# Optimization experiments

Hardware: AMD Instinct MI355X
Metric: run time of the kernel (lower is better)

## Reference

```python
import jax, jax.numpy as jnp
import numpy as np

N_NODES = 50000
N_EDGES = 800000


def setup_inputs() -> dict:
    key = jax.random.key(0)
    ks = jax.random.split(key, 8)
    x = jax.random.normal(ks[0], (N_NODES, 128), dtype=jnp.float32)
    edge_index = jax.random.randint(ks[1], (2, N_EDGES), 0, N_NODES, dtype=jnp.int64)
    # Glorot-ish scaled weights (GCNConv uses glorot init)
    W1 = jax.random.normal(ks[2], (128, 128), dtype=jnp.float32) * 0.08
    W2 = jax.random.normal(ks[3], (128, 128), dtype=jnp.float32) * 0.08
    W3 = jax.random.normal(ks[4], (128, 64), dtype=jnp.float32) * 0.08
    b1 = jnp.zeros((128,), jnp.float32)
    b2 = jnp.zeros((128,), jnp.float32)
    b3 = jnp.zeros((64,), jnp.float32)
    return {"x": x, "W1": W1, "b1": b1, "W2": W2, "b2": b2,
            "W3": W3, "b3": b3, "edge_index": edge_index}


def _gcn_layer(x, W, b, src, dst, norm, n):
    # GCNConv: out = D^{-1/2} (A+I) D^{-1/2} (x W) + b
    h = x @ W                                   # [N, F_out]
    msg = h[src] * norm[:, None]                # gather + scale per edge
    agg = jax.ops.segment_sum(msg, dst, num_segments=n)  # scatter-add
    return agg + b


def reference(x, W1, b1, W2, b2, W3, b3, edge_index):
    n = x.shape[0]
    loops = jnp.arange(n, dtype=edge_index.dtype)
    src = jnp.concatenate([edge_index[0], loops])  # add self-loops (PyG default)
    dst = jnp.concatenate([edge_index[1], loops])
    # symmetric normalization from in-degree (incl. self-loops)
    deg = jax.ops.segment_sum(jnp.ones_like(dst, dtype=x.dtype), dst, num_segments=n)
    dis = jnp.where(deg > 0, jax.lax.rsqrt(deg), 0.0)
    norm = dis[src] * dis[dst]                   # [E+N]

    h = jax.nn.relu(_gcn_layer(x, W1, b1, src, dst, norm, n))
    # dropout(p=0.5) is identity in eval mode
    h = jax.nn.relu(_gcn_layer(h, W2, b2, src, dst, norm, n))
    h = _gcn_layer(h, W3, b3, src, dst, norm, n)
    return jax.nn.log_softmax(h, axis=1)
```

## Files before the change

### kernel.cpp

```cpp
#include <hip/hip_runtime.h>
#include <hip/hip_bf16.h>
#include <cstdint>

typedef unsigned int uint32;
typedef unsigned short ushort16;

#define EPB 4096

__device__ inline uint32 pack_bf16(float a, float b) {
    uint32 ua = __float_as_uint(a);
    ua += 0x7fff + ((ua >> 16) & 1);
    uint32 ub = __float_as_uint(b);
    ub += 0x7fff + ((ub >> 16) & 1);
    return (ua >> 16) | (ub & 0xffff0000u);
}
__device__ inline float bf_lo(uint32 w) { return __uint_as_float(w << 16); }
__device__ inline float bf_hi(uint32 w) { return __uint_as_float(w & 0xffff0000u); }


__global__ void k_init_i32(int* __restrict__ p, int n) {
    int i = blockIdx.x * blockDim.x + threadIdx.x;
    if (i < n) p[i] = 0;
}

__global__ __launch_bounds__(256) void k_bhist(const int* __restrict__ dstv,
                                               int* __restrict__ bhist, int e, int shift) {
    __shared__ int h[256];
    int t = threadIdx.x;
    h[t] = 0;
    __syncthreads();
    int b0 = blockIdx.x * EPB;
#pragma unroll
    for (int i = 0; i < EPB / 256; ++i) {
        int idx = b0 + i * 256 + t;
        if (idx < e) atomicAdd(&h[dstv[idx] >> shift], 1);
    }
    __syncthreads();
    if (h[t]) atomicAdd(&bhist[t], h[t]);
}

__global__ __launch_bounds__(256) void k_bscan(const int* __restrict__ bhist,
                                               int* __restrict__ bpre, int* __restrict__ bcur,
                                               int nb, int e) {
    __shared__ int s[256];
    int t = threadIdx.x;
    int v = (t < nb) ? bhist[t] : 0;
    s[t] = v;
    __syncthreads();
    for (int off = 1; off < 256; off <<= 1) {
        int a = (t >= off) ? s[t - off] : 0;
        __syncthreads();
        s[t] += a;
        __syncthreads();
    }
    if (t < nb) { bpre[t] = s[t] - v; bcur[t] = s[t] - v; }
    if (t == 0) bpre[nb] = e;
}

__global__ __launch_bounds__(256) void k_partition(const int* __restrict__ srcv,
                                                   const int* __restrict__ dstv,
                                                   int* __restrict__ bcur,
                                                   uint2* __restrict__ pairs,
                                                   int e, int shift) {
    __shared__ int h[256], base[256], cur[256];
    int t = threadIdx.x;
    h[t] = 0; cur[t] = 0;
    __syncthreads();
    int s[EPB / 256], d[EPB / 256];
    int b0 = blockIdx.x * EPB;
#pragma unroll
    for (int i = 0; i < EPB / 256; ++i) {
        int idx = b0 + i * 256 + t;
        if (idx < e) {
            s[i] = srcv[idx]; d[i] = dstv[idx];
            atomicAdd(&h[d[i] >> shift], 1);
        } else d[i] = -1;
    }
    __syncthreads();
    if (h[t]) base[t] = atomicAdd(&bcur[t], h[t]);
    __syncthreads();
#pragma unroll
    for (int i = 0; i < EPB / 256; ++i) {
        if (d[i] >= 0) {
            int b = d[i] >> shift;
            int sl = atomicAdd(&cur[b], 1);
            pairs[base[b] + sl] = make_uint2((unsigned)s[i], (unsigned)d[i]);
        }
    }
}

__global__ __launch_bounds__(256) void k_bcount(const uint2* __restrict__ pairs,
                                                const int* __restrict__ bpre,
                                                int* __restrict__ cnt, int n, int shift) {
    __shared__ int c[1024];
    int t = threadIdx.x;
    int win = 1 << shift;
    for (int i = t; i < win; i += 256) c[i] = 0;
    __syncthreads();
    int wb = blockIdx.x << shift;
    int e0 = bpre[blockIdx.x], e1 = bpre[blockIdx.x + 1];
    for (int i = e0 + t; i < e1; i += 256) {
        uint2 p = pairs[i];
        atomicAdd(&c[(int)p.y - wb], 1);
    }
    __syncthreads();
    for (int i = t; i < win; i += 256) if (wb + i < n) cnt[wb + i] = c[i];
}

__global__ __launch_bounds__(256) void k_bfill(const uint2* __restrict__ pairs,
                                               const int* __restrict__ bpre,
                                               const int* __restrict__ rp,
                                               int* __restrict__ col, int shift) {
    __shared__ int c[1024];
    int t = threadIdx.x;
    int win = 1 << shift;
    for (int i = t; i < win; i += 256) c[i] = 0;
    __syncthreads();
    int wb = blockIdx.x << shift;
    int e0 = bpre[blockIdx.x], e1 = bpre[blockIdx.x + 1];
    for (int i = e0 + t; i < e1; i += 256) {
        uint2 p = pairs[i];
        int sl = atomicAdd(&c[(int)p.y - wb], 1);
        col[rp[p.y] + sl] = (int)p.x;
    }
}

__global__ void k_dis(const int* __restrict__ cnt, float* __restrict__ dis, int n) {
    int i = blockIdx.x * blockDim.x + threadIdx.x;
    if (i < n) dis[i] = rsqrtf((float)(cnt[i] + 1));
}


__global__ __launch_bounds__(256) void k_partial_sums(const int* __restrict__ cnt,
                                                      int* __restrict__ partial, int n) {
    int base = blockIdx.x * 1024 + threadIdx.x * 4;
    int4 v = make_int4(0, 0, 0, 0);
    if (base + 3 < n) v = *(const int4*)(cnt + base);
    else {
        if (base + 0 < n) v.x = cnt[base + 0];
        if (base + 1 < n) v.y = cnt[base + 1];
        if (base + 2 < n) v.z = cnt[base + 2];
    }
    int s = v.x + v.y + v.z + v.w;
    for (int off = 32; off; off >>= 1) s += __shfl_xor(s, off, 64);
    __shared__ int wsum[4];
    int lane = threadIdx.x & 63, wid = threadIdx.x >> 6;
    if (lane == 0) wsum[wid] = s;
    __syncthreads();
    if (threadIdx.x == 0) partial[blockIdx.x] = wsum[0] + wsum[1] + wsum[2] + wsum[3];
}

__global__ __launch_bounds__(1024) void k_scan_partials(int* __restrict__ partial, int nb,
                                                        int* __restrict__ rp, int n, int etot) {
    __shared__ int s[1024];
    int t = threadIdx.x;
    int v = (t < nb) ? partial[t] : 0;
    s[t] = v;
    __syncthreads();
    for (int off = 1; off < 1024; off <<= 1) {
        int add = (t >= off) ? s[t - off] : 0;
        __syncthreads();
        s[t] += add;
        __syncthreads();
    }
    if (t < nb) partial[t] = s[t] - v;
    if (t == 0) rp[n] = etot;
}

__global__ __launch_bounds__(256) void k_local_scan(const int* __restrict__ cnt,
                                                    const int* __restrict__ partial,
                                                    int* __restrict__ rp, int n) {
    int base = blockIdx.x * 1024 + threadIdx.x * 4;
    int4 v = make_int4(0, 0, 0, 0);
    if (base + 3 < n) v = *(const int4*)(cnt + base);
    else {
        if (base + 0 < n) v.x = cnt[base + 0];
        if (base + 1 < n) v.y = cnt[base + 1];
        if (base + 2 < n) v.z = cnt[base + 2];
    }
    int tsum = v.x + v.y + v.z + v.w;
    int lane = threadIdx.x & 63, wid = threadIdx.x >> 6;
    int inc = tsum;
    for (int off = 1; off < 64; off <<= 1) {
        int y = __shfl_up(inc, off, 64);
        if (lane >= off) inc += y;
    }
    int exc = inc - tsum;
    __shared__ int wtot[4];
    if (lane == 63) wtot[wid] = inc;
    __syncthreads();
    int woff = 0;
    for (int w = 0; w < wid; ++w) woff += wtot[w];
    int p0 = partial[blockIdx.x] + woff + exc;
    int p1 = p0 + v.x, p2 = p1 + v.y, p3 = p2 + v.z;
    if (base + 3 < n) {
        *(int4*)&rp[base] = make_int4(p0, p1, p2, p3);
    } else {
        if (base + 0 < n) rp[base + 0] = p0;
        if (base + 1 < n) rp[base + 1] = p1;
        if (base + 2 < n) rp[base + 2] = p2;
    }
}


template <int FOUT>
__global__ __launch_bounds__(FOUT * 2) void k_gemm_scale(
        const float* __restrict__ X, const float* __restrict__ W,
        const float* __restrict__ dis, uint32* __restrict__ Yb, int n) {
    constexpr int CT = FOUT / 4;
    constexpr int NT = CT * 8;
    __shared__ float xs[32][132];
    __shared__ float ws[32 * FOUT];
    int tid = threadIdx.x;
    int ct = tid % CT, rt = tid / CT;
    int row0 = blockIdx.x * 32;
    float acc[4][4] = {};

    for (int kt = 0; kt < 4; ++kt) {
        for (int e = tid; e < 256; e += NT) {
            int r = e >> 3, kq = (e & 7) << 2;
            int row = min(row0 + r, n - 1);
            float4 v = *(const float4*)(X + (size_t)row * 128 + kt * 32 + kq);
            *(float4*)&xs[r][kq] = v;
        }
        for (int e = tid; e < 32 * FOUT / 4; e += NT) {
            *(float4*)&ws[e * 4] = *(const float4*)&W[kt * 32 * FOUT + e * 4];
        }
        __syncthreads();
#pragma unroll 8
        for (int k = 0; k < 32; ++k) {
            float4 bv = *(const float4*)&ws[k * FOUT + ct * 4];
            float a0 = xs[rt * 4 + 0][k];
            float a1 = xs[rt * 4 + 1][k];
            float a2 = xs[rt * 4 + 2][k];
            float a3 = xs[rt * 4 + 3][k];
            acc[0][0] += a0 * bv.x; acc[0][1] += a0 * bv.y; acc[0][2] += a0 * bv.z; acc[0][3] += a0 * bv.w;
            acc[1][0] += a1 * bv.x; acc[1][1] += a1 * bv.y; acc[1][2] += a1 * bv.z; acc[1][3] += a1 * bv.w;
            acc[2][0] += a2 * bv.x; acc[2][1] += a2 * bv.y; acc[2][2] += a2 * bv.z; acc[2][3] += a2 * bv.w;
            acc[3][0] += a3 * bv.x; acc[3][1] += a3 * bv.y; acc[3][2] += a3 * bv.z; acc[3][3] += a3 * bv.w;
        }
        __syncthreads();
    }
    for (int i = 0; i < 4; ++i) {
        int row = row0 + rt * 4 + i;
        if (row < n) {
            float d = dis[row];
            uint2 o;
            o.x = pack_bf16(acc[i][0] * d, acc[i][1] * d);
            o.y = pack_bf16(acc[i][2] * d, acc[i][3] * d);
            *(uint2*)&Yb[(size_t)row * (FOUT / 2) + ct * 2] = o;
        }
    }
}


__global__ __launch_bounds__(256) void k_agg_relu128(
        const uint32* __restrict__ hb, const int* __restrict__ rp,
        const int* __restrict__ col, const float* __restrict__ dis,
        const float* __restrict__ bias, float* __restrict__ out, int n) {
    int wid = threadIdx.x >> 6;
    int lane = threadIdx.x & 63;
    int v = blockIdx.x * 4 + wid;
    if (v >= n) return;
    uint32 mv = hb[(size_t)v * 64 + lane];
    float ax = bf_lo(mv), ay = bf_hi(mv);
    int s = __builtin_amdgcn_readfirstlane(rp[v]);
    int e = __builtin_amdgcn_readfirstlane(rp[v + 1]);
    int k = s;
    for (; k + 16 <= e; k += 16) {
        uint32 m[16];
#pragma unroll
        for (int j = 0; j < 16; ++j) {
            int u = col[k + j];
            m[j] = hb[(size_t)u * 64 + lane];
        }
#pragma unroll
        for (int j = 0; j < 16; ++j) { ax += bf_lo(m[j]); ay += bf_hi(m[j]); }
    }
    if (k + 8 <= e) {
        uint32 m[8];
#pragma unroll
        for (int j = 0; j < 8; ++j) m[j] = hb[(size_t)col[k + j] * 64 + lane];
#pragma unroll
        for (int j = 0; j < 8; ++j) { ax += bf_lo(m[j]); ay += bf_hi(m[j]); }
        k += 8;
    }
    if (k + 4 <= e) {
        uint32 m[4];
#pragma unroll
        for (int j = 0; j < 4; ++j) m[j] = hb[(size_t)col[k + j] * 64 + lane];
#pragma unroll
        for (int j = 0; j < 4; ++j) { ax += bf_lo(m[j]); ay += bf_hi(m[j]); }
        k += 4;
    }
    for (; k < e; ++k) {
        uint32 m = hb[(size_t)col[k] * 64 + lane];
        ax += bf_lo(m); ay += bf_hi(m);
    }
    float d = dis[v];
    float2 b = ((const float2*)bias)[lane];
    float ox = fmaxf(d * ax + b.x, 0.f);
    float oy = fmaxf(d * ay + b.y, 0.f);
    ((float2*)out)[(size_t)v * 64 + lane] = make_float2(ox, oy);
}

__global__ __launch_bounds__(256) void k_agg_lsm64(
        const ushort16* __restrict__ hb, const int* __restrict__ rp,
        const int* __restrict__ col, const float* __restrict__ dis,
        const float* __restrict__ bias, float* __restrict__ out, int n) {
    int wid = threadIdx.x >> 6;
    int lane = threadIdx.x & 63;
    int v = blockIdx.x * 4 + wid;
    if (v >= n) return;
    float acc = __uint_as_float((uint32)hb[(size_t)v * 64 + lane] << 16);
    int s = __builtin_amdgcn_readfirstlane(rp[v]);
    int e = __builtin_amdgcn_readfirstlane(rp[v + 1]);
    int k = s;
    for (; k + 16 <= e; k += 16) {
        ushort16 m[16];
#pragma unroll
        for (int j = 0; j < 16; ++j) m[j] = hb[(size_t)col[k + j] * 64 + lane];
#pragma unroll
        for (int j = 0; j < 16; ++j) acc += __uint_as_float((uint32)m[j] << 16);
    }
    if (k + 8 <= e) {
        ushort16 m[8];
#pragma unroll
        for (int j = 0; j < 8; ++j) m[j] = hb[(size_t)col[k + j] * 64 + lane];
#pragma unroll
        for (int j = 0; j < 8; ++j) acc += __uint_as_float((uint32)m[j] << 16);
        k += 8;
    }
    for (; k < e; ++k) acc += __uint_as_float((uint32)hb[(size_t)col[k] * 64 + lane] << 16);
    float val = dis[v] * acc + bias[lane];
    float m = val;
    for (int off = 32; off; off >>= 1) m = fmaxf(m, __shfl_xor(m, off, 64));
    float ex = expf(val - m);
    float ss = ex;
    for (int off = 32; off; off >>= 1) ss += __shfl_xor(ss, off, 64);
    out[(size_t)v * 64 + lane] = val - m - logf(ss);
}


extern "C" void kernel_launch(void* const* d_in, const int* in_sizes, int n_in,
                              void* d_out, int out_size, void* d_ws, size_t ws_size,
                              hipStream_t stream) {
    const float* x  = (const float*)d_in[0];
    const float* W1 = (const float*)d_in[1];
    const float* b1 = (const float*)d_in[2];
    const float* W2 = (const float*)d_in[3];
    const float* b2 = (const float*)d_in[4];
    const float* W3 = (const float*)d_in[5];
    const float* b3 = (const float*)d_in[6];
    const int*   ei = (const int*)d_in[7];

    const int N = in_sizes[0] / 128;
    const int E = in_sizes[7] / 2;
    const int* srcv = ei;
    const int* dstv = ei + E;

    int shift = 8;
    while (((N + (1 << shift) - 1) >> shift) > 256) ++shift;
    const int NB  = (N + (1 << shift) - 1) >> shift;

    char* ws = (char*)d_ws;
    size_t off = 0;
    auto alloc = [&](size_t bytes) -> void* {
        void* p = ws + off;
        off += (bytes + 255) & ~(size_t)255;
        return p;
    };
    float*  dis   = (float*)alloc((size_t)N * 4);
    int*    cnt   = (int*)alloc((size_t)N * 4);
    int*    rp    = (int*)alloc((size_t)(N + 1) * 4);
    int*    col   = (int*)alloc((size_t)E * 4);
    int*    part  = (int*)alloc((size_t)1024 * 4);
    int*    bhist = (int*)alloc((size_t)(NB + 1) * 4);
    int*    bpre  = (int*)alloc((size_t)(NB + 1) * 4);
    int*    bcur  = (int*)alloc((size_t)(NB + 1) * 4);
    uint2*  pairs = (uint2*)alloc((size_t)E * 8);
    uint32* hsb   = (uint32*)alloc((size_t)N * 128 * 2);
    float*  bufF  = (float*)alloc((size_t)N * 128 * 4);
    float*  outp  = (float*)d_out;

    const int tb = 256;
    const int nbE = (E + EPB - 1) / EPB;
    const int nbS = (N + 1023) / 1024;

    k_init_i32<<<(NB + tb - 1) / tb, tb, 0, stream>>>(bhist, NB);
    k_bhist<<<nbE, 256, 0, stream>>>(dstv, bhist, E, shift);
    k_bscan<<<1, 256, 0, stream>>>(bhist, bpre, bcur, NB, E);
    k_partition<<<nbE, 256, 0, stream>>>(srcv, dstv, bcur, pairs, E, shift);
    k_bcount<<<NB, 256, 0, stream>>>(pairs, bpre, cnt, N, shift);
    k_dis<<<(N + tb - 1) / tb, tb, 0, stream>>>(cnt, dis, N);
    k_partial_sums<<<nbS, 256, 0, stream>>>(cnt, part, N);
    k_scan_partials<<<1, 1024, 0, stream>>>(part, nbS, rp, N, E);
    k_local_scan<<<nbS, 256, 0, stream>>>(cnt, part, rp, N);
    k_bfill<<<NB, 256, 0, stream>>>(pairs, bpre, rp, col, shift);

    int gblk = (N + 31) / 32;
    int ablk = (N + 3) / 4;
    k_gemm_scale<128><<<gblk, 256, 0, stream>>>(x, W1, dis, hsb, N);
    k_agg_relu128<<<ablk, 256, 0, stream>>>(hsb, rp, col, dis, b1, bufF, N);
    k_gemm_scale<128><<<gblk, 256, 0, stream>>>(bufF, W2, dis, hsb, N);
    k_agg_relu128<<<ablk, 256, 0, stream>>>(hsb, rp, col, dis, b2, bufF, N);
    k_gemm_scale<64><<<gblk, 128, 0, stream>>>(bufF, W3, dis, hsb, N);
    k_agg_lsm64<<<ablk, 256, 0, stream>>>((const ushort16*)hsb, rp, col, dis, b3, outp, N);
}
```

Measured before the change: 230.1 us.

## Use bf16 MFMA GEMMs, bf16 intermediates, and fuse CSR build into one kernel

Replaces the fp32 shared-memory GEMM with a bf16 MFMA 16x16x32 kernel that reads pre-transposed bf16 weights. The aggregation kernels now write bf16 activations instead of fp32, which halves intermediate traffic. The per-node count, degree, three-stage prefix scan and column fill are merged into a single per-bucket kernel that uses a local scan. The bucket shift is fixed at 8, which assumes N ≤ 65536, and the bf16 layer inputs lower precision.

```diff
diff --git a/kernel.cpp b/kernel.cpp
--- a/kernel.cpp
+++ b/kernel.cpp
@@ -3,16 +3,18 @@
 #include <cstdint>
 
 typedef unsigned int uint32;
-typedef unsigned short ushort16;
+typedef __attribute__((ext_vector_type(8))) short short8;
+typedef __attribute__((ext_vector_type(4))) float f32x4;
 
 #define EPB 4096
 
+__device__ inline unsigned short bf16r(float f) {
+    uint32 u = __float_as_uint(f);
+    u += 0x7fff + ((u >> 16) & 1);
+    return (unsigned short)(u >> 16);
+}
 __device__ inline uint32 pack_bf16(float a, float b) {
-    uint32 ua = __float_as_uint(a);
-    ua += 0x7fff + ((ua >> 16) & 1);
-    uint32 ub = __float_as_uint(b);
-    ub += 0x7fff + ((ub >> 16) & 1);
-    return (ua >> 16) | (ub & 0xffff0000u);
+    return (uint32)bf16r(a) | ((uint32)bf16r(b) << 16);
 }
 __device__ inline float bf_lo(uint32 w) { return __uint_as_float(w << 16); }
 __device__ inline float bf_hi(uint32 w) { return __uint_as_float(w & 0xffff0000u); }
@@ -24,7 +26,7 @@
 }
 
 __global__ __launch_bounds__(256) void k_bhist(const int* __restrict__ dstv,
-                                               int* __restrict__ bhist, int e, int shift) {
+                                               int* __restrict__ bhist, int e) {
     __shared__ int h[256];
     int t = threadIdx.x;
     h[t] = 0;
@@ -33,7 +35,7 @@
 #pragma unroll
     for (int i = 0; i < EPB / 256; ++i) {
         int idx = b0 + i * 256 + t;
-        if (idx < e) atomicAdd(&h[dstv[idx] >> shift], 1);
+        if (idx < e) atomicAdd(&h[dstv[idx] >> 8], 1);
     }
     __syncthreads();
     if (h[t]) atomicAdd(&bhist[t], h[t]);
@@ -41,7 +43,7 @@
 
 __global__ __launch_bounds__(256) void k_bscan(const int* __restrict__ bhist,
                                                int* __restrict__ bpre, int* __restrict__ bcur,
-                                               int nb, int e) {
+                                               int nb, int e, int* __restrict__ rp, int n) {
     __shared__ int s[256];
     int t = threadIdx.x;
     int v = (t < nb) ? bhist[t] : 0;
@@ -54,14 +56,13 @@
         __syncthreads();
     }
     if (t < nb) { bpre[t] = s[t] - v; bcur[t] = s[t] - v; }
-    if (t == 0) bpre[nb] = e;
+    if (t == 0) { bpre[nb] = e; rp[n] = e; }
 }
 
 __global__ __launch_bounds__(256) void k_partition(const int* __restrict__ srcv,
                                                    const int* __restrict__ dstv,
                                                    int* __restrict__ bcur,
-                                                   uint2* __restrict__ pairs,
-                                                   int e, int shift) {
+                                                   uint2* __restrict__ pairs, int e) {
     __shared__ int h[256], base[256], cur[256];
     int t = threadIdx.x;
     h[t] = 0; cur[t] = 0;
@@ -73,7 +74,7 @@
         int idx = b0 + i * 256 + t;
         if (idx < e) {
             s[i] = srcv[idx]; d[i] = dstv[idx];
-            atomicAdd(&h[d[i] >> shift], 1);
+            atomicAdd(&h[d[i] >> 8], 1);
         } else d[i] = -1;
     }
     __syncthreads();
@@ -82,173 +83,116 @@
 #pragma unroll
     for (int i = 0; i < EPB / 256; ++i) {
         if (d[i] >= 0) {
-            int b = d[i] >> shift;
+            int b = d[i] >> 8;
             int sl = atomicAdd(&cur[b], 1);
             pairs[base[b] + sl] = make_uint2((unsigned)s[i], (unsigned)d[i]);
         }
     }
 }
 
-__global__ __launch_bounds__(256) void k_bcount(const uint2* __restrict__ pairs,
-                                                const int* __restrict__ bpre,
-                                                int* __restrict__ cnt, int n, int shift) {
-    __shared__ int c[1024];
+__global__ __launch_bounds__(256) void k_bfinish(const uint2* __restrict__ pairs,
+                                                 const int* __restrict__ bpre,
+                                                 int* __restrict__ rp, float* __restrict__ dis,
+                                                 int* __restrict__ col, int n) {
+    __shared__ int c[256], sc[256], cur[256];
     int t = threadIdx.x;
-    int win = 1 << shift;
-    for (int i = t; i < win; i += 256) c[i] = 0;
-    __syncthreads();
-    int wb = blockIdx.x << shift;
+    c[t] = 0; cur[t] = 0;
+    __syncthreads();
+    int wb = blockIdx.x << 8;
     int e0 = bpre[blockIdx.x], e1 = bpre[blockIdx.x + 1];
+    for (int i = e0 + t; i < e1; i += 256) atomicAdd(&c[(int)pairs[i].y - wb], 1);
+    __syncthreads();
+    int own = c[t];
+    sc[t] = own;
+    __syncthreads();
+    for (int off = 1; off < 256; off <<= 1) {
+        int a = (t >= off) ? sc[t - off] : 0;
+        __syncthreads();
+        sc[t] += a;
+        __syncthreads();
+    }
+    int base = bpre[blockIdx.x] + sc[t] - own;
+    __syncthreads();
+    sc[t] = base;
+    int v = wb + t;
+    if (v < n) { rp[v] = base; dis[v] = rsqrtf((float)(own + 1)); }
+    __syncthreads();
     for (int i = e0 + t; i < e1; i += 256) {
         uint2 p = pairs[i];
-        atomicAdd(&c[(int)p.y - wb], 1);
-    }
-    __syncthreads();
-    for (int i = t; i < win; i += 256) if (wb + i < n) cnt[wb + i] = c[i];
-}
-
-__global__ __launch_bounds__(256) void k_bfill(const uint2* __restrict__ pairs,
-                                               const int* __restrict__ bpre,
-                                               const int* __restrict__ rp,
-                                               int* __restrict__ col, int shift) {
-    __shared__ int c[1024];
-    int t = threadIdx.x;
-    int win = 1 << shift;
-    for (int i = t; i < win; i += 256) c[i] = 0;
-    __syncthreads();
-    int wb = blockIdx.x << shift;
-    int e0 = bpre[blockIdx.x], e1 = bpre[blockIdx.x + 1];
-    for (int i = e0 + t; i < e1; i += 256) {
-        uint2 p = pairs[i];
-        int sl = atomicAdd(&c[(int)p.y - wb], 1);
-        col[rp[p.y] + sl] = (int)p.x;
-    }
-}
-
-__global__ void k_dis(const int* __restrict__ cnt, float* __restrict__ dis, int n) {
-    int i = blockIdx.x * blockDim.x + threadIdx.x;
-    if (i < n) dis[i] = rsqrtf((float)(cnt[i] + 1));
-}
-
-
-__global__ __launch_bounds__(256) void k_partial_sums(const int* __restrict__ cnt,
-                                                      int* __restrict__ partial, int n) {
-    int base = blockIdx.x * 1024 + threadIdx.x * 4;
-    int4 v = make_int4(0, 0, 0, 0);
-    if (base + 3 < n) v = *(const int4*)(cnt + base);
-    else {
-        if (base + 0 < n) v.x = cnt[base + 0];
-        if (base + 1 < n) v.y = cnt[base + 1];
-        if (base + 2 < n) v.z = cnt[base + 2];
-    }
-    int s = v.x + v.y + v.z + v.w;
-    for (int off = 32; off; off >>= 1) s += __shfl_xor(s, off, 64);
-    __shared__ int wsum[4];
-    int lane = threadIdx.x & 63, wid = threadIdx.x >> 6;
-    if (lane == 0) wsum[wid] = s;
-    __syncthreads();
-    if (threadIdx.x == 0) partial[blockIdx.x] = wsum[0] + wsum[1] + wsum[2] + wsum[3];
-}
-
-__global__ __launch_bounds__(1024) void k_scan_partials(int* __restrict__ partial, int nb,
-                                                        int* __restrict__ rp, int n, int etot) {
-    __shared__ int s[1024];
-    int t = threadIdx.x;
-    int v = (t < nb) ? partial[t] : 0;
-    s[t] = v;
-    __syncthreads();
-    for (int off = 1; off < 1024; off <<= 1) {
-        int add = (t >= off) ? s[t - off] : 0;
-        __syncthreads();
-        s[t] += add;
-        __syncthreads();
-    }
-    if (t < nb) partial[t] = s[t] - v;
-    if (t == 0) rp[n] = etot;
-}
-
-__global__ __launch_bounds__(256) void k_local_scan(const int* __restrict__ cnt,
-                                                    const int* __restrict__ partial,
-                                                    int* __restrict__ rp, int n) {
-    int base = blockIdx.x * 1024 + threadIdx.x * 4;
-    int4 v = make_int4(0, 0, 0, 0);
-    if (base + 3 < n) v = *(const int4*)(cnt + base);
-    else {
-        if (base + 0 < n) v.x = cnt[base + 0];
-        if (base + 1 < n) v.y = cnt[base + 1];
-        if (base + 2 < n) v.z = cnt[base + 2];
-    }
-    int tsum = v.x + v.y + v.z + v.w;
-    int lane = threadIdx.x & 63, wid = threadIdx.x >> 6;
-    int inc = tsum;
-    for (int off = 1; off < 64; off <<= 1) {
-        int y = __shfl_up(inc, off, 64);
-        if (lane >= off) inc += y;
-    }
-    int exc = inc - tsum;
-    __shared__ int wtot[4];
-    if (lane == 63) wtot[wid] = inc;
-    __syncthreads();
-    int woff = 0;
-    for (int w = 0; w < wid; ++w) woff += wtot[w];
-    int p0 = partial[blockIdx.x] + woff + exc;
-    int p1 = p0 + v.x, p2 = p1 + v.y, p3 = p2 + v.z;
-    if (base + 3 < n) {
-        *(int4*)&rp[base] = make_int4(p0, p1, p2, p3);
+        int bl = (int)p.y - wb;
+        int sl = atomicAdd(&cur[bl], 1);
+        col[sc[bl] + sl] = (int)p.x;
+    }
+}
+
+
+__global__ __launch_bounds__(256) void k_wprep(const float* __restrict__ W1,
+                                               const float* __restrict__ W2,
+                                               const float* __restrict__ W3,
+                                               unsigned short* __restrict__ Wt1,
+                                               unsigned short* __restrict__ Wt2,
+                                               unsigned short* __restrict__ Wt3) {
+    const float* W = blockIdx.x == 0 ? W1 : (blockIdx.x == 1 ? W2 : W3);
+    unsigned short* Wt = blockIdx.x == 0 ? Wt1 : (blockIdx.x == 1 ? Wt2 : Wt3);
+    int F = blockIdx.x == 2 ? 64 : 128;
+    for (int i = threadIdx.x; i < 128 * F; i += 256) {
+        int k = i / F, c = i % F;
+        Wt[c * 128 + k] = bf16r(W[i]);
+    }
+}
+
+
+template <int FOUT, bool BF16IN>
+__global__ __launch_bounds__(256) void k_gemm_mfma(
+        const void* __restrict__ Xv, const unsigned short* __restrict__ Wt,
+        const float* __restrict__ dis, unsigned short* __restrict__ Yb, int n) {
+    constexpr int CT = FOUT / 16;
+    int lane = threadIdx.x & 63;
+    int wv = threadIdx.x >> 6;
+    int r16 = lane & 15, kg = lane >> 4;
+    int rowA = blockIdx.x * 64 + wv * 16 + r16;
+    int ra = min(rowA, n - 1);
+    short8 afr[4];
+    if (BF16IN) {
+        const unsigned short* Xb = (const unsigned short*)Xv;
+#pragma unroll
+        for (int ks = 0; ks < 4; ++ks)
+            afr[ks] = *(const short8*)(Xb + (size_t)ra * 128 + ks * 32 + kg * 8);
     } else {
-        if (base + 0 < n) rp[base + 0] = p0;
-        if (base + 1 < n) rp[base + 1] = p1;
-        if (base + 2 < n) rp[base + 2] = p2;
-    }
-}
-
-
-template <int FOUT>
-__global__ __launch_bounds__(FOUT * 2) void k_gemm_scale(
-        const float* __restrict__ X, const float* __restrict__ W,
-        const float* __restrict__ dis, uint32* __restrict__ Yb, int n) {
-    constexpr int CT = FOUT / 4;
-    constexpr int NT = CT * 8;
-    __shared__ float xs[32][132];
-    __shared__ float ws[32 * FOUT];
-    int tid = threadIdx.x;
-    int ct = tid % CT, rt = tid / CT;
-    int row0 = blockIdx.x * 32;
-    float acc[4][4] = {};
-
-    for (int kt = 0; kt < 4; ++kt) {
-        for (int e = tid; e < 256; e += NT) {
-            int r = e >> 3, kq = (e & 7) << 2;
-            int row = min(row0 + r, n - 1);
-            float4 v = *(const float4*)(X + (size_t)row * 128 + kt * 32 + kq);
-            *(float4*)&xs[r][kq] = v;
-        }
-        for (int e = tid; e < 32 * FOUT / 4; e += NT) {
-            *(float4*)&ws[e * 4] = *(const float4*)&W[kt * 32 * FOUT + e * 4];
-        }
-        __syncthreads();
-#pragma unroll 8
-        for (int k = 0; k < 32; ++k) {
-            float4 bv = *(const float4*)&ws[k * FOUT + ct * 4];
-            float a0 = xs[rt * 4 + 0][k];
-            float a1 = xs[rt * 4 + 1][k];
-            float a2 = xs[rt * 4 + 2][k];
-            float a3 = xs[rt * 4 + 3][k];
-            acc[0][0] += a0 * bv.x; acc[0][1] += a0 * bv.y; acc[0][2] += a0 * bv.z; acc[0][3] += a0 * bv.w;
-            acc[1][0] += a1 * bv.x; acc[1][1] += a1 * bv.y; acc[1][2] += a1 * bv.z; acc[1][3] += a1 * bv.w;
-            acc[2][0] += a2 * bv.x; acc[2][1] += a2 * bv.y; acc[2][2] += a2 * bv.z; acc[2][3] += a2 * bv.w;
-            acc[3][0] += a3 * bv.x; acc[3][1] += a3 * bv.y; acc[3][2] += a3 * bv.z; acc[3][3] += a3 * bv.w;
-        }
-        __syncthreads();
-    }
-    for (int i = 0; i < 4; ++i) {
-        int row = row0 + rt * 4 + i;
+        const float* Xf = (const float*)Xv;
+#pragma unroll
+        for (int ks = 0; ks < 4; ++ks) {
+            const float* p = Xf + (size_t)ra * 128 + ks * 32 + kg * 8;
+            float4 f0 = *(const float4*)p;
+            float4 f1 = *(const float4*)(p + 4);
+            short8 a;
+            a[0] = (short)bf16r(f0.x); a[1] = (short)bf16r(f0.y);
+            a[2] = (short)bf16r(f0.z); a[3] = (short)bf16r(f0.w);
+            a[4] = (short)bf16r(f1.x); a[5] = (short)bf16r(f1.y);
+            a[6] = (short)bf16r(f1.z); a[7] = (short)bf16r(f1.w);
+            afr[ks] = a;
+        }
+    }
+    f32x4 acc[CT];
+#pragma unroll
+    for (int c = 0; c < CT; ++c) acc[c] = (f32x4){0.f, 0.f, 0.f, 0.f};
+#pragma unroll
+    for (int ks = 0; ks < 4; ++ks) {
+#pragma unroll
+        for (int c = 0; c < CT; ++c) {
+            short8 b = *(const short8*)(Wt + (c * 16 + r16) * 128 + ks * 32 + kg * 8);
+            acc[c] = __builtin_amdgcn_mfma_f32_16x16x32_bf16(afr[ks], b, acc[c], 0, 0, 0);
+        }
+    }
+    int rbase = blockIdx.x * 64 + wv * 16 + kg * 4;
+#pragma unroll
+    for (int j = 0; j < 4; ++j) {
+        int row = rbase + j;
         if (row < n) {
             float d = dis[row];
-            uint2 o;
-            o.x = pack_bf16(acc[i][0] * d, acc[i][1] * d);
-            o.y = pack_bf16(acc[i][2] * d, acc[i][3] * d);
-            *(uint2*)&Yb[(size_t)row * (FOUT / 2) + ct * 2] = o;
+#pragma unroll
+            for (int c = 0; c < CT; ++c)
+                Yb[(size_t)row * FOUT + c * 16 + r16] = bf16r(acc[c][j] * d);
         }
     }
 }
@@ -257,7 +201,7 @@
 __global__ __launch_bounds__(256) void k_agg_relu128(
         const uint32* __restrict__ hb, const int* __restrict__ rp,
         const int* __restrict__ col, const float* __restrict__ dis,
-        const float* __restrict__ bias, float* __restrict__ out, int n) {
+        const float* __restrict__ bias, uint32* __restrict__ outb, int n) {
     int wid = threadIdx.x >> 6;
     int lane = threadIdx.x & 63;
     int v = blockIdx.x * 4 + wid;
@@ -301,11 +245,11 @@
     float2 b = ((const float2*)bias)[lane];
     float ox = fmaxf(d * ax + b.x, 0.f);
     float oy = fmaxf(d * ay + b.y, 0.f);
-    ((float2*)out)[(size_t)v * 64 + lane] = make_float2(ox, oy);
+    outb[(size_t)v * 64 + lane] = pack_bf16(ox, oy);
 }
 
 __global__ __launch_bounds__(256) void k_agg_lsm64(
-        const ushort16* __restrict__ hb, const int* __restrict__ rp,
+        const unsigned short* __restrict__ hb, const int* __restrict__ rp,
         const int* __restrict__ col, const float* __restrict__ dis,
         const float* __restrict__ bias, float* __restrict__ out, int n) {
     int wid = threadIdx.x >> 6;
@@ -317,14 +261,14 @@
     int e = __builtin_amdgcn_readfirstlane(rp[v + 1]);
     int k = s;
     for (; k + 16 <= e; k += 16) {
-        ushort16 m[16];
+        unsigned short m[16];
 #pragma unroll
         for (int j = 0; j < 16; ++j) m[j] = hb[(size_t)col[k + j] * 64 + lane];
 #pragma unroll
         for (int j = 0; j < 16; ++j) acc += __uint_as_float((uint32)m[j] << 16);
     }
     if (k + 8 <= e) {
-        ushort16 m[8];
+        unsigned short m[8];
 #pragma unroll
         for (int j = 0; j < 8; ++j) m[j] = hb[(size_t)col[k + j] * 64 + lane];
 #pragma unroll
@@ -358,10 +302,7 @@
     const int E = in_sizes[7] / 2;
     const int* srcv = ei;
     const int* dstv = ei + E;
-
-    int shift = 8;
-    while (((N + (1 << shift) - 1) >> shift) > 256) ++shift;
-    const int NB  = (N + (1 << shift) - 1) >> shift;
+    const int NB = (N + 255) >> 8;
 
     char* ws = (char*)d_ws;
     size_t off = 0;
@@ -370,40 +311,36 @@
         off += (bytes + 255) & ~(size_t)255;
         return p;
     };
-    float*  dis   = (float*)alloc((size_t)N * 4);
-    int*    cnt   = (int*)alloc((size_t)N * 4);
-    int*    rp    = (int*)alloc((size_t)(N + 1) * 4);
-    int*    col   = (int*)alloc((size_t)E * 4);
-    int*    part  = (int*)alloc((size_t)1024 * 4);
-    int*    bhist = (int*)alloc((size_t)(NB + 1) * 4);
-    int*    bpre  = (int*)alloc((size_t)(NB + 1) * 4);
-    int*    bcur  = (int*)alloc((size_t)(NB + 1) * 4);
-    uint2*  pairs = (uint2*)alloc((size_t)E * 8);
-    uint32* hsb   = (uint32*)alloc((size_t)N * 128 * 2);
-    float*  bufF  = (float*)alloc((size_t)N * 128 * 4);
-    float*  outp  = (float*)d_out;
+    float*          dis   = (float*)alloc((size_t)N * 4);
+    int*            rp    = (int*)alloc((size_t)(N + 1) * 4);
+    int*            col   = (int*)alloc((size_t)E * 4);
+    int*            bhist = (int*)alloc((size_t)(NB + 1) * 4);
+    int*            bpre  = (int*)alloc((size_t)(NB + 1) * 4);
+    int*            bcur  = (int*)alloc((size_t)(NB + 1) * 4);
+    uint2*          pairs = (uint2*)alloc((size_t)E * 8);
+    unsigned short* Wt1   = (unsigned short*)alloc(128 * 128 * 2);
+    unsigned short* Wt2   = (unsigned short*)alloc(128 * 128 * 2);
+    unsigned short* Wt3   = (unsigned short*)alloc(64 * 128 * 2);
+    unsigned short* hsb   = (unsigned short*)alloc((size_t)N * 128 * 2);
+    unsigned short* hbX   = (unsigned short*)alloc((size_t)N * 128 * 2);
+    float*          outp  = (float*)d_out;
 
     const int tb = 256;
     const int nbE = (E + EPB - 1) / EPB;
-    const int nbS = (N + 1023) / 1024;
 
     k_init_i32<<<(NB + tb - 1) / tb, tb, 0, stream>>>(bhist, NB);
-    k_bhist<<<nbE, 256, 0, stream>>>(dstv, bhist, E, shift);
-    k_bscan<<<1, 256, 0, stream>>>(bhist, bpre, bcur, NB, E);
-    k_partition<<<nbE, 256, 0, stream>>>(srcv, dstv, bcur, pairs, E, shift);
-    k_bcount<<<NB, 256, 0, stream>>>(pairs, bpre, cnt, N, shift);
-    k_dis<<<(N + tb - 1) / tb, tb, 0, stream>>>(cnt, dis, N);
-    k_partial_sums<<<nbS, 256, 0, stream>>>(cnt, part, N);
-    k_scan_partials<<<1, 1024, 0, stream>>>(part, nbS, rp, N, E);
-    k_local_scan<<<nbS, 256, 0, stream>>>(cnt, part, rp, N);
-    k_bfill<<<NB, 256, 0, stream>>>(pairs, bpre, rp, col, shift);
-
-    int gblk = (N + 31) / 32;
+    k_bhist<<<nbE, 256, 0, stream>>>(dstv, bhist, E);
+    k_bscan<<<1, 256, 0, stream>>>(bhist, bpre, bcur, NB, E, rp, N);
+    k_partition<<<nbE, 256, 0, stream>>>(srcv, dstv, bcur, pairs, E);
+    k_bfinish<<<NB, 256, 0, stream>>>(pairs, bpre, rp, dis, col, N);
+    k_wprep<<<3, 256, 0, stream>>>(W1, W2, W3, Wt1, Wt2, Wt3);
+
+    int gblk = (N + 63) / 64;
     int ablk = (N + 3) / 4;
-    k_gemm_scale<128><<<gblk, 256, 0, stream>>>(x, W1, dis, hsb, N);
-    k_agg_relu128<<<ablk, 256, 0, stream>>>(hsb, rp, col, dis, b1, bufF, N);
-    k_gemm_scale<128><<<gblk, 256, 0, stream>>>(bufF, W2, dis, hsb, N);
-    k_agg_relu128<<<ablk, 256, 0, stream>>>(hsb, rp, col, dis, b2, bufF, N);
-    k_gemm_scale<64><<<gblk, 128, 0, stream>>>(bufF, W3, dis, hsb, N);
-    k_agg_lsm64<<<ablk, 256, 0, stream>>>((const ushort16*)hsb, rp, col, dis, b3, outp, N);
-}
+    k_gemm_mfma<128, false><<<gblk, 256, 0, stream>>>(x, Wt1, dis, hsb, N);
+    k_agg_relu128<<<ablk, 256, 0, stream>>>((const uint32*)hsb, rp, col, dis, b1, (uint32*)hbX, N);
+    k_gemm_mfma<128, true><<<gblk, 256, 0, stream>>>(hbX, Wt2, dis, hsb, N);
+    k_agg_relu128<<<ablk, 256, 0, stream>>>((const uint32*)hsb, rp, col, dis, b2, (uint32*)hbX, N);
+    k_gemm_mfma<64, true><<<gblk, 256, 0, stream>>>(hbX, Wt3, dis, hsb, N);
+    k_agg_lsm64<<<ablk, 256, 0, stream>>>(hsb, rp, col, dis, b3, outp, N);
+}
```

Result: faster. 207.7 us (-9.7%).
